# Kernel optimization log

Measured on AMD Instinct MI355X. Metric: run time of the kernel, lower is better.

The kernel has to match this reference:

```python
import jax, jax.numpy as jnp
import numpy as np

T, B, U, A, H, K, G = 800, 128, 64, 64, 256, 10, 20
IN1, IN2, IN3 = 3 + A, 3 + A + H, 3 + A + H


def _lstm_cell(x, h, c, W_ih, W_hh, b):
    # PyTorch LSTMCell: gates in order i, f, g, o
    z = x @ W_ih.T + h @ W_hh.T + b
    i, f, g, o = jnp.split(z, 4, axis=-1)
    c_new = jax.nn.sigmoid(f) * c + jax.nn.sigmoid(i) * jnp.tanh(g)
    h_new = jax.nn.sigmoid(o) * jnp.tanh(c_new)
    return h_new, c_new


def setup_inputs() -> dict:
    key = jax.random.key(0)
    ks = jax.random.split(key, 32)
    s = 0.08
    p = {}
    p['x'] = jax.random.normal(ks[0], (T, B, 3), jnp.float32)
    p['c'] = jax.random.uniform(ks[1], (B, U, A), jnp.float32)
    p['W1_ih'] = jax.random.normal(ks[2], (4 * H, IN1), jnp.float32) * s
    p['W1_hh'] = jax.random.normal(ks[3], (4 * H, H), jnp.float32) * s
    p['b1'] = jax.random.normal(ks[4], (4 * H,), jnp.float32) * s
    p['W2_ih'] = jax.random.normal(ks[5], (4 * H, IN2), jnp.float32) * s
    p['W2_hh'] = jax.random.normal(ks[6], (4 * H, H), jnp.float32) * s
    p['b2'] = jax.random.normal(ks[7], (4 * H,), jnp.float32) * s
    p['W3_ih'] = jax.random.normal(ks[8], (4 * H, IN3), jnp.float32) * s
    p['W3_hh'] = jax.random.normal(ks[9], (4 * H, H), jnp.float32) * s
    p['b3'] = jax.random.normal(ks[10], (4 * H,), jnp.float32) * s
    p['Ww'] = jax.random.normal(ks[11], (3 * K, H), jnp.float32) * s
    p['bw'] = jax.random.normal(ks[12], (3 * K,), jnp.float32) * s
    p['We'] = jax.random.normal(ks[13], (1, H), jnp.float32) * s
    p['be'] = jax.random.normal(ks[14], (1,), jnp.float32) * s
    p['Wpi'] = jax.random.normal(ks[15], (G, H), jnp.float32) * s
    p['bpi'] = jax.random.normal(ks[16], (G,), jnp.float32) * s
    p['Wm1'] = jax.random.normal(ks[17], (G, H), jnp.float32) * s
    p['bm1'] = jax.random.normal(ks[18], (G,), jnp.float32) * s
    p['Wm2'] = jax.random.normal(ks[19], (G, H), jnp.float32) * s
    p['bm2'] = jax.random.normal(ks[20], (G,), jnp.float32) * s
    p['Ws1'] = jax.random.normal(ks[21], (G, H), jnp.float32) * s
    p['bs1'] = jax.random.normal(ks[22], (G,), jnp.float32) * s
    p['Ws2'] = jax.random.normal(ks[23], (G, H), jnp.float32) * s
    p['bs2'] = jax.random.normal(ks[24], (G,), jnp.float32) * s
    p['Wr'] = jax.random.normal(ks[25], (G, H), jnp.float32) * s
    p['br'] = jax.random.normal(ks[26], (G,), jnp.float32) * s
    return p


def reference(x, c, W1_ih, W1_hh, b1, W2_ih, W2_hh, b2, W3_ih, W3_hh, b3,
              Ww, bw, We, be, Wpi, bpi, Wm1, bm1, Wm2, bm2,
              Ws1, bs1, Ws2, bs2, Wr, br):
    u = jnp.arange(U, dtype=x.dtype)  # character positions

    def step(carry, x_t):
        h1, c1, h2, c2, h3, c3, w, kappa = carry
        h1, c1 = _lstm_cell(jnp.concatenate([x_t, w], 1), h1, c1, W1_ih, W1_hh, b1)
        win = jnp.exp(h1 @ Ww.T + bw)                     # [B, 3K]
        alpha, beta, k = jnp.split(win, 3, axis=1)
        kappa = 0.1 * k + kappa                           # [B, K]
        # Phi[b,u] = sum_k alpha * exp(-beta * (kappa - u)^2)
        d = kappa[:, None, :] - u[None, :, None]          # [B, U, K]
        phi = jnp.sum(alpha[:, None, :] * jnp.exp(-beta[:, None, :] * d * d), -1)  # [B, U]
        w = jnp.einsum('bu,bua->ba', phi, c)              # [B, A]
        h2, c2 = _lstm_cell(jnp.concatenate([x_t, w, h1], 1), h2, c2, W2_ih, W2_hh, b2)
        h3, c3 = _lstm_cell(jnp.concatenate([x_t, w, h2], 1), h3, c3, W3_ih, W3_hh, b3)
        return (h1, c1, h2, c2, h3, c3, w, kappa), h3

    z = jnp.zeros((B, H), x.dtype)
    init = (z, z, z, z, z, z, jnp.ones((B, A), x.dtype), jnp.zeros((B, K), x.dtype))
    _, out = jax.lax.scan(step, init, x)                  # out: [T, B, H]

    es = jax.nn.sigmoid(-(out @ We.T + be)).squeeze(-1)   # 1/(1+exp(z)) == sigmoid(-z)
    pis = jax.nn.softmax(out @ Wpi.T + bpi, axis=2)
    mu1s = out @ Wm1.T + bm1
    mu2s = out @ Wm2.T + bm2
    sigma1s = jnp.exp(out @ Ws1.T + bs1)
    sigma2s = jnp.exp(out @ Ws2.T + bs2)
    rhos = jnp.tanh(out @ Wr.T + br)
    return es, pis, mu1s, mu2s, sigma1s, sigma2s, rhos
```

## Files before the change

### kernel.cpp

```cpp
#include <hip/hip_runtime.h>
#include <utility>

#define TT 800
#define BB 128
#define HH 256
#define UU 64
#define AA 64
#define KK 10
#define GG 20
#define NWG 256
#define GB 32
#define NGRP 4

typedef float f32x4 __attribute__((ext_vector_type(4)));
typedef __bf16 bf16y8 __attribute__((ext_vector_type(8)));
typedef short bf16s8 __attribute__((ext_vector_type(8)));
typedef unsigned long long u64x2 __attribute__((ext_vector_type(2)));

__device__ __forceinline__ float bf2f(unsigned short u) {
  return __uint_as_float(((unsigned int)u) << 16);
}
__device__ __forceinline__ unsigned short f2bf(float f) {
  unsigned int x = __float_as_uint(f);
  x += 0x7FFFu + ((x >> 16) & 1u);
  return (unsigned short)(x >> 16);
}
__device__ __forceinline__ unsigned packf(float v) {
  unsigned short hi = f2bf(v);
  unsigned short lo = f2bf(v - bf2f(hi));
  return (unsigned)hi | ((unsigned)lo << 16);
}
__device__ __forceinline__ float unpackf(unsigned u) {
  return bf2f((unsigned short)(u & 0xFFFF)) + bf2f((unsigned short)(u >> 16));
}
__device__ __forceinline__ float sigm(float x) { return 1.0f / (1.0f + __expf(-x)); }
__device__ __forceinline__ float rin(const void* p, size_t i, bool f32) {
  return f32 ? ((const float*)p)[i] : bf2f(((const unsigned short*)p)[i]);
}
__device__ __forceinline__ bf16y8 ld8(const unsigned short* p) {
  return __builtin_bit_cast(bf16y8, *(const bf16s8*)p);
}

__device__ __forceinline__ unsigned ald(const unsigned* p) {
  return __hip_atomic_load(p, __ATOMIC_RELAXED, __HIP_MEMORY_SCOPE_AGENT);
}
__device__ __forceinline__ void ast(unsigned* p, unsigned v) {
  __hip_atomic_store(p, v, __ATOMIC_RELAXED, __HIP_MEMORY_SCOPE_AGENT);
}

__device__ __forceinline__ void ld16(u64x2& d, const unsigned* p) {
  asm volatile("global_load_dwordx4 %0, %1, off sc0 sc1" : "=v"(d) : "v"(p));
}
template <int N>
__device__ __forceinline__ void waitvm() {
  asm volatile("s_waitcnt vmcnt(%0)" :: "i"(N) : "memory");
  __builtin_amdgcn_sched_barrier(0);
}

template <typename F, int... I>
__device__ __forceinline__ void unroll_seq(F&& f, std::integer_sequence<int, I...>) {
  (f(std::integral_constant<int, I>{}), ...);
}


struct KArgs {
  const void* in[27];
  float* out;
  float* kappa;
  unsigned *xu;
  unsigned *wu;
  unsigned *h1[2], *h2[2], *h3[2];
  unsigned* bar;
};

__device__ void fillB(unsigned short* Bhi, unsigned short* Blo, const void* Wih,
                      const void* Whh, int KP, int ihCols, int ihEnd, int hhStart,
                      int q, int tid, bool f32) {
  int total = KP * 16;
  for (int idx = tid; idx < total; idx += 256) {
    int k = idx >> 4, n = idx & 15;
    int row = (n >> 2) * HH + q * 4 + (n & 3);
    float v = 0.f;
    if (k < 3) v = rin(Wih, (size_t)row * ihCols + k, f32);
    else if (k >= 8 && k < ihEnd) v = rin(Wih, (size_t)row * ihCols + (k - 5), f32);
    else if (k >= hhStart && k < hhStart + 256) v = rin(Whh, (size_t)row * HH + (k - hhStart), f32);
    unsigned short hi = f2bf(v);
    int a = ((k >> 3) * 16 + n) * 8 + (k & 7);
    Bhi[a] = hi;
    Blo[a] = f2bf(v - bf2f(hi));
  }
}

template <int KC, bool R3, int WB>
__device__ __forceinline__ void gate_mfma(
    const unsigned* __restrict__ xt, const unsigned* __restrict__ wu,
    const unsigned* __restrict__ r2, const unsigned* __restrict__ r3,
    const unsigned* __restrict__ dz,
    const unsigned short* __restrict__ Bhi, const unsigned short* __restrict__ Blo,
    const float* __restrict__ bias4, float& creg, unsigned* __restrict__ hout,
    int grp, int q, float* zls, int tid) {
  const int wave = tid >> 6, lane = tid & 63;
  if ((wave >> 1) != (WB >> 1)) return;
  const int wv = wave & 1;
  const int n15 = lane & 15, quad = lane >> 4;
  const int b = grp * GB + wv * 16 + n15;

  unsigned xv0 = 0, xv1 = 0, xv2 = 0;
  if (quad == 0) {
    xv0 = xt[b * 3 + 0];
    xv1 = xt[b * 3 + 1];
    xv2 = xt[b * 3 + 2];
  }
  asm volatile("" :: "v"(xv0), "v"(xv1), "v"(xv2));

  constexpr int DEP = 12;
  u64x2 buf[DEP][2];

  auto addr = [&](int kc) -> const unsigned* {
    const int k0 = kc * 32 + quad * 8;
    if (kc == 0 && quad == 0) return dz;
    if (k0 < 72) return wu + ((k0 - 8) >> 3) * 1024 + b * 8;
    if (k0 < 328) return r2 + ((k0 - 72) >> 3) * 1024 + b * 8;
    if (R3 && k0 < 584) return r3 + ((k0 - 328) >> 3) * 1024 + b * 8;
    return dz;
  };
  auto issue = [&](int kc, int slot) {
    const unsigned* p = addr(kc);
    ld16(buf[slot][0], p);
    ld16(buf[slot][1], p + 4);
  };

#pragma unroll
  for (int kc = 0; kc < DEP && kc < KC; ++kc) issue(kc, kc);

  f32x4 acc = {0.f, 0.f, 0.f, 0.f};

  unroll_seq([&](auto kcc) {
    constexpr int kc = decltype(kcc)::value;
    constexpr int end = (kc + DEP < KC) ? (kc + DEP) : KC;
    waitvm<2 * (end - kc - 1)>();
    u64x2* sp = buf[kc % DEP];
    unsigned long long s[4] = { sp[0][0], sp[0][1], sp[1][0], sp[1][1] };
    bf16s8 th, tl;
#pragma unroll
    for (int j = 0; j < 4; ++j) {
      unsigned lo32 = (unsigned)s[j], hi32 = (unsigned)(s[j] >> 32);
      th[2 * j] = (short)(lo32 & 0xFFFFu);     tl[2 * j] = (short)(lo32 >> 16);
      th[2 * j + 1] = (short)(hi32 & 0xFFFFu); tl[2 * j + 1] = (short)(hi32 >> 16);
    }
    if constexpr (kc == 0) {
      if (quad == 0) {
        th[0] = (short)(xv0 & 0xFFFFu); tl[0] = (short)(xv0 >> 16);
        th[1] = (short)(xv1 & 0xFFFFu); tl[1] = (short)(xv1 >> 16);
        th[2] = (short)(xv2 & 0xFFFFu); tl[2] = (short)(xv2 >> 16);
      }
    }
    bf16y8 ah = __builtin_bit_cast(bf16y8, th);
    bf16y8 al = __builtin_bit_cast(bf16y8, tl);
    const int boff = ((kc * 4 + quad) * 16 + n15) * 8;
    bf16y8 bh = ld8(Bhi + boff), bl = ld8(Blo + boff);
    acc = __builtin_amdgcn_mfma_f32_16x16x32_bf16(ah, bh, acc, 0, 0, 0);
    acc = __builtin_amdgcn_mfma_f32_16x16x32_bf16(ah, bl, acc, 0, 0, 0);
    acc = __builtin_amdgcn_mfma_f32_16x16x32_bf16(al, bh, acc, 0, 0, 0);
    if constexpr (kc + DEP < KC) issue(kc + DEP, kc % DEP);
  }, std::make_integer_sequence<int, KC>{});

  float* zw = zls + wave * (16 * 17);
#pragma unroll
  for (int r = 0; r < 4; ++r) zw[(quad * 4 + r) * 17 + n15] = acc[r];
  const int m = lane >> 2, j = lane & 3;
  const int hu = q * 4 + j;
  const int bb = grp * GB + wv * 16 + m;
  float zi = zw[m * 17 + (0 + j)]  + bias4[0];
  float zf = zw[m * 17 + (4 + j)]  + bias4[1];
  float zg = zw[m * 17 + (8 + j)]  + bias4[2];
  float zo = zw[m * 17 + (12 + j)] + bias4[3];
  float cn = sigm(zf) * creg + sigm(zi) * tanhf(zg);
  creg = cn;
  float hn = sigm(zo) * tanhf(cn);
  ast(hout + (hu >> 3) * 1024 + bb * 8 + (hu & 7), packf(hn));
}

template <bool F32>
__device__ void window_stage(const KArgs& a, int b, const unsigned* __restrict__ h1c,
                             int tid, float* misc) {
  float* slab = misc;
  float* part = misc + 264;
  float* win  = misc + 508;
  float* kap  = misc + 538;
  float* phi  = misc + 552;
  const int wave = tid >> 6, lane = tid & 63;
  if (wave == 0) {
    const unsigned* p = h1c + (lane >> 1) * 1024 + b * 8 + (lane & 1) * 4;
    u64x2 d;
    ld16(d, p);
    waitvm<0>();
    const int hu0 = (lane >> 1) * 8 + (lane & 1) * 4;
    float* s4 = slab + (hu0 >> 5) * 33 + (hu0 & 31);
    s4[0] = unpackf((unsigned)d[0]);
    s4[1] = unpackf((unsigned)(d[0] >> 32));
    s4[2] = unpackf((unsigned)d[1]);
    s4[3] = unpackf((unsigned)(d[1] >> 32));
  }
  __syncthreads();
  if (tid < 240) {
    int r = tid >> 3, pp = tid & 7;
    const float* hh = slab + pp * 33;
    float s = 0.f;
    if (F32) {
      const f32x4* w4 = (const f32x4*)((const float*)a.in[11] + (size_t)r * HH + pp * 32);
#pragma unroll
      for (int j = 0; j < 8; ++j) {
        f32x4 v = w4[j];
        s += v[0] * hh[4 * j];     s += v[1] * hh[4 * j + 1];
        s += v[2] * hh[4 * j + 2]; s += v[3] * hh[4 * j + 3];
      }
    } else {
      const unsigned short* wr = (const unsigned short*)a.in[11] + (size_t)r * HH + pp * 32;
#pragma unroll
      for (int j = 0; j < 4; ++j) {
        bf16s8 v = *(const bf16s8*)(wr + 8 * j);
#pragma unroll
        for (int e = 0; e < 8; ++e) s += bf2f((unsigned short)v[e]) * hh[8 * j + e];
      }
    }
    part[tid] = s;
  }
  __syncthreads();
  if (tid < 30) {
    float s = rin(a.in[12], tid, F32);
#pragma unroll
    for (int i = 0; i < 8; ++i) s += part[tid * 8 + i];
    win[tid] = __expf(s);
  }
  __syncthreads();
  if (tid < 10) {
    float kp = a.kappa[b * KK + tid] + 0.1f * win[20 + tid];
    a.kappa[b * KK + tid] = kp;
    kap[tid] = kp;
  }
  __syncthreads();
  if (tid < 64) {
    float u = (float)tid, s = 0.f;
#pragma unroll
    for (int r = 0; r < 10; ++r) {
      float d = kap[r] - u;
      s += win[r] * __expf(-win[10 + r] * d * d);
    }
    phi[tid] = s;
  }
  __syncthreads();
  if (tid < 64) {
    float s = 0.f;
    for (int u = 0; u < 64; ++u) s += phi[u] * rin(a.in[1], ((size_t)b * UU + u) * AA + tid, F32);
    ast(a.wu + (tid >> 3) * 1024 + b * 8 + (tid & 7), packf(s));
  }
}

template <bool F32>
__device__ void proj_stage(const KArgs& a, int tt, const unsigned* __restrict__ h3b,
                           int b, int tid, float* misc) {
  float* shm  = misc;
  float* part = misc + 256;
  float* zp   = misc + 500;
  const int wave = tid >> 6, lane = tid & 63;
  if (wave == 0) {
    const unsigned* p = h3b + (lane >> 1) * 1024 + b * 8 + (lane & 1) * 4;
    u64x2 d;
    ld16(d, p);
    waitvm<0>();
    const int hu0 = (lane >> 1) * 8 + (lane & 1) * 4;
    shm[hu0 + 0] = unpackf((unsigned)d[0]);
    shm[hu0 + 1] = unpackf((unsigned)(d[0] >> 32));
    shm[hu0 + 2] = unpackf((unsigned)d[1]);
    shm[hu0 + 3] = unpackf((unsigned)(d[1] >> 32));
  }
  __syncthreads();
  if (tid < 242) {
    int o = tid >> 1, hf = tid & 1;
    const void* Wt;
    const void* bt;
    int rr;
    if (o == 0) {
      Wt = a.in[13]; bt = a.in[14]; rr = 0;
    } else {
      int fam = (o - 1) / 20;
      rr = (o - 1) % 20;
      Wt = a.in[15 + fam * 2];
      bt = a.in[16 + fam * 2];
    }
    float s0 = hf ? 0.f : rin(bt, rr, F32), s1 = 0.f;
    const float* hh = shm + hf * 128;
    if (F32) {
      const f32x4* w4 = (const f32x4*)((const float*)Wt + (size_t)rr * HH + hf * 128);
#pragma unroll 8
      for (int j = 0; j < 32; ++j) {
        f32x4 v = w4[j];
        s0 += v[0] * hh[4 * j];     s1 += v[1] * hh[4 * j + 1];
        s0 += v[2] * hh[4 * j + 2]; s1 += v[3] * hh[4 * j + 3];
      }
    } else {
      const unsigned short* wr = (const unsigned short*)Wt + (size_t)rr * HH + hf * 128;
#pragma unroll 4
      for (int j = 0; j < 16; ++j) {
        bf16s8 v = *(const bf16s8*)(wr + 8 * j);
#pragma unroll
        for (int e = 0; e < 8; e += 2) {
          s0 += bf2f((unsigned short)v[e]) * hh[8 * j + e];
          s1 += bf2f((unsigned short)v[e + 1]) * hh[8 * j + e + 1];
        }
      }
    }
    part[tid] = s0 + s1;
  }
  __syncthreads();
  if (tid < 121) zp[tid] = part[tid * 2] + part[tid * 2 + 1];
  __syncthreads();
  size_t tb = (size_t)tt * BB + b;
  if (tid == 0) {
    a.out[tb] = 1.f / (1.f + __expf(zp[0]));
  } else if (tid < 121) {
    int fam = (tid - 1) / 20, g = (tid - 1) % 20;
    float z = zp[tid];
    float val;
    if (fam == 0) {
      float mx = -1e30f;
      for (int jj = 0; jj < 20; ++jj) mx = fmaxf(mx, zp[1 + jj]);
      float den = 0.f;
      for (int jj = 0; jj < 20; ++jj) den += __expf(zp[1 + jj] - mx);
      val = __expf(z - mx) / den;
    } else if (fam <= 2) {
      val = z;
    } else if (fam <= 4) {
      val = __expf(z);
    } else {
      val = tanhf(z);
    }
    a.out[(size_t)102400 + (size_t)fam * 2048000 + tb * GG + g] = val;
  }
}

#define BAR_WORDS (256 + NWG * 32)

__global__ void __launch_bounds__(256) bar_init_kernel(unsigned* bar) {
  for (int i = threadIdx.x; i < BAR_WORDS; i += 256) bar[i] = 0u;
}

__global__ void __launch_bounds__(256, 1) hsm_kernel(KArgs a) {
  __shared__ unsigned short B1h[5632], B1l[5632];
  __shared__ unsigned short B2h[9728], B2l[9728];
  __shared__ unsigned short B3h[9728], B3l[9728];
  __shared__ float zls[4 * 16 * 17];
  __shared__ float misc[768];
  __shared__ unsigned islast;

  const int tid = threadIdx.x;
  const int wg = blockIdx.x;
  const int grp = wg >> 6;
  const int q = wg & 63;
  unsigned* cnt_full = a.bar;
  unsigned* cnt_grp  = a.bar + 32 * (1 + grp);
  unsigned* flags    = a.bar + 256;
  unsigned* myflag   = flags + wg * 32;
  const unsigned* dz = a.bar + 160;

  auto barrier = [&](unsigned* cnt, unsigned target, unsigned fv, int nfl, int flbase) {
    __syncthreads();
    if (tid == 0) {
      unsigned old = __hip_atomic_fetch_add(cnt, 1u, __ATOMIC_RELAXED,
                                            __HIP_MEMORY_SCOPE_AGENT);
      islast = (old == target - 1u) ? 1u : 0u;
    }
    __syncthreads();
    if (islast) {
      if (tid < nfl) ast(flags + (flbase + tid) * 32, fv);
    } else if (tid == 0) {
      while (ald(myflag) < fv) __builtin_amdgcn_s_sleep(2);
    }
    __syncthreads();
  };

  bool isf32;
  {
    const unsigned short* w = (const unsigned short*)a.in[3];
    int cnt = 0;
    for (int i = 0; i < 128; ++i) {
      float v = bf2f(w[i]);
      if (!(fabsf(v) <= 100.f)) cnt++;
    }
    isf32 = (cnt > 0);
  }

  const int g0 = wg * 256 + tid, gs = 65536;
  if (isf32) {
    const float* xp = (const float*)a.in[0];
    for (int i = g0; i < 307200; i += gs) ast(a.xu + i, packf(xp[i]));
  } else {
    const unsigned short* xp = (const unsigned short*)a.in[0];
    for (int i = g0; i < 307200; i += gs) ast(a.xu + i, (unsigned)xp[i]);
  }
  if (g0 < 32768) {
    ast(a.h1[0] + g0, 0u); ast(a.h1[1] + g0, 0u);
    ast(a.h2[0] + g0, 0u); ast(a.h2[1] + g0, 0u);
    ast(a.h3[0] + g0, 0u); ast(a.h3[1] + g0, 0u);
  }
  if (g0 < 8192) ast(a.wu + g0, 0x00003F80u);
  if (q < GB && tid < KK) a.kappa[(grp * GB + q) * KK + tid] = 0.f;

  float bs1[4], bs2[4], bs3[4];
  {
    const int hu = q * 4 + (tid & 3);
#pragma unroll
    for (int g = 0; g < 4; ++g) {
      bs1[g] = rin(a.in[4], g * HH + hu, isf32);
      bs2[g] = rin(a.in[7], g * HH + hu, isf32);
      bs3[g] = rin(a.in[10], g * HH + hu, isf32);
    }
  }
  float c1r = 0.f, c2r = 0.f, c3r = 0.f;

  fillB(B1h, B1l, a.in[2], a.in[3], 352, 67, 72, 72, q, tid, isf32);
  fillB(B2h, B2l, a.in[5], a.in[6], 608, 323, 328, 328, q, tid, isf32);
  fillB(B3h, B3l, a.in[8], a.in[9], 608, 323, 328, 328, q, tid, isf32);
  barrier(cnt_full, NWG, 1, NWG, 0);

  unsigned ph = 0;

  gate_mfma<11, false, 2>(a.xu, a.wu, a.h1[0], nullptr, dz, B1h, B1l, bs1, c1r,
                          a.h1[1], grp, q, zls, tid);
  ++ph; barrier(cnt_grp, ph * 64u, ph + 1u, 64, grp * 64);

  for (int t = 0; t < TT; ++t) {
    const int p = t & 1;
    const unsigned* xt = a.xu + (size_t)t * BB * 3;
    if (q < GB) {
      if (isf32) window_stage<true>(a, grp * GB + q, a.h1[1 - p], tid, misc);
      else       window_stage<false>(a, grp * GB + q, a.h1[1 - p], tid, misc);
    } else if (t > 0) {
      if (isf32) proj_stage<true>(a, t - 1, a.h3[p], grp * GB + q - GB, tid, misc);
      else       proj_stage<false>(a, t - 1, a.h3[p], grp * GB + q - GB, tid, misc);
    }
    ++ph; barrier(cnt_grp, ph * 64u, ph + 1u, 64, grp * 64);
    gate_mfma<19, true, 0>(xt, a.wu, a.h1[1 - p], a.h2[p], dz, B2h, B2l,
                           bs2, c2r, a.h2[1 - p], grp, q, zls, tid);
    ++ph; barrier(cnt_grp, ph * 64u, ph + 1u, 64, grp * 64);
    gate_mfma<19, true, 0>(xt, a.wu, a.h2[1 - p], a.h3[p], dz, B3h, B3l,
                           bs3, c3r, a.h3[1 - p], grp, q, zls, tid);
    if (t < TT - 1) {
      gate_mfma<11, false, 2>(xt + BB * 3, a.wu, a.h1[1 - p], nullptr, dz,
                              B1h, B1l, bs1, c1r, a.h1[p], grp, q, zls, tid);
    }
    ++ph; barrier(cnt_grp, ph * 64u, ph + 1u, 64, grp * 64);
  }
  if (q >= GB) {
    if (isf32) proj_stage<true>(a, TT - 1, a.h3[0], grp * GB + q - GB, tid, misc);
    else       proj_stage<false>(a, TT - 1, a.h3[0], grp * GB + q - GB, tid, misc);
  }
}

extern "C" void kernel_launch(void* const* d_in, const int* in_sizes, int n_in,
                              void* d_out, int out_size, void* d_ws, size_t ws_size,
                              hipStream_t stream) {
  KArgs a;
  for (int i = 0; i < 27; ++i) a.in[i] = d_in[i];
  a.out = (float*)d_out;

  char* ws = (char*)d_ws;
  size_t off = 0;
  auto take = [&](size_t bytes) {
    void* p = ws + off;
    off = (off + bytes + 127) & ~(size_t)127;
    return p;
  };
  a.kappa = (float*)take(1280 * 4);
  a.wu    = (unsigned*)take(8192 * 4);
  a.h1[0] = (unsigned*)take(32768 * 4);
  a.h1[1] = (unsigned*)take(32768 * 4);
  a.h2[0] = (unsigned*)take(32768 * 4);
  a.h2[1] = (unsigned*)take(32768 * 4);
  a.h3[0] = (unsigned*)take(32768 * 4);
  a.h3[1] = (unsigned*)take(32768 * 4);
  a.xu    = (unsigned*)take(307200 * 4);
  a.bar   = (unsigned*)take(BAR_WORDS * 4);

  bar_init_kernel<<<1, 256, 0, stream>>>(a.bar);
  hsm_kernel<<<NWG, 256, 0, stream>>>(a);
}
```

Baseline: 12.71 ms.

## Replace group barrier before layer-2 gates with per-window-block flag waits

Window blocks now publish a per-block step flag once they finish computing w. The layer-2 gate routine becomes a variant that first prefetches the h1 and h2 operand chunks, then spins only on the 32 window flags of its group before loading the w-dependent chunks. This removes one full group barrier per timestep and overlaps the h1/h2 loads with the wait. The cost is more polling traffic on the flags and a flag area added to the barrier buffer. Proj-stage blocks are no longer fenced at this point, so correctness depends on layer 2 not reading their outputs.

```diff
diff --git a/kernel.cpp b/kernel.cpp
--- a/kernel.cpp
+++ b/kernel.cpp
@@ -163,6 +163,114 @@
     acc = __builtin_amdgcn_mfma_f32_16x16x32_bf16(ah, bl, acc, 0, 0, 0);
     acc = __builtin_amdgcn_mfma_f32_16x16x32_bf16(al, bh, acc, 0, 0, 0);
     if constexpr (kc + DEP < KC) issue(kc + DEP, kc % DEP);
+  }, std::make_integer_sequence<int, KC>{});
+
+  float* zw = zls + wave * (16 * 17);
+#pragma unroll
+  for (int r = 0; r < 4; ++r) zw[(quad * 4 + r) * 17 + n15] = acc[r];
+  const int m = lane >> 2, j = lane & 3;
+  const int hu = q * 4 + j;
+  const int bb = grp * GB + wv * 16 + m;
+  float zi = zw[m * 17 + (0 + j)]  + bias4[0];
+  float zf = zw[m * 17 + (4 + j)]  + bias4[1];
+  float zg = zw[m * 17 + (8 + j)]  + bias4[2];
+  float zo = zw[m * 17 + (12 + j)] + bias4[3];
+  float cn = sigm(zf) * creg + sigm(zi) * tanhf(zg);
+  creg = cn;
+  float hn = sigm(zo) * tanhf(cn);
+  ast(hout + (hu >> 3) * 1024 + bb * 8 + (hu & 7), packf(hn));
+}
+
+template <int kc> constexpr int lw_wait() {
+  return kc == 0 ? 4 : kc == 1 ? 2 : kc == 2 ? 0 :
+         kc == 15 ? 6 : kc == 16 ? 4 : kc == 17 ? 2 : kc == 18 ? 0 : -1;
+}
+__device__ __forceinline__ void gate_mfma_lw(
+    const unsigned* __restrict__ xt, const unsigned* __restrict__ wu,
+    const unsigned* __restrict__ r2, const unsigned* __restrict__ r3,
+    const unsigned* __restrict__ dz,
+    const unsigned short* __restrict__ Bhi, const unsigned short* __restrict__ Blo,
+    const float* __restrict__ bias4, float& creg, unsigned* __restrict__ hout,
+    const unsigned* __restrict__ afl, unsigned tgt,
+    int grp, int q, float* zls, int tid) {
+  constexpr int KC = 19, DEP = 12;
+  const int wave = tid >> 6, lane = tid & 63;
+  if (wave >= 2) return;
+  const int wv = wave & 1;
+  const int n15 = lane & 15, quad = lane >> 4;
+  const int b = grp * GB + wv * 16 + n15;
+
+  unsigned xv0 = 0, xv1 = 0, xv2 = 0;
+  if (quad == 0) {
+    xv0 = xt[b * 3 + 0];
+    xv1 = xt[b * 3 + 1];
+    xv2 = xt[b * 3 + 2];
+  }
+  asm volatile("" :: "v"(xv0), "v"(xv1), "v"(xv2));
+
+  u64x2 buf[DEP][2];
+  u64x2 wbuf[3][2];
+
+  auto addr = [&](int kc) -> const unsigned* {
+    const int k0 = kc * 32 + quad * 8;
+    if (kc == 0 && quad == 0) return dz;
+    if (k0 < 72) return wu + ((k0 - 8) >> 3) * 1024 + b * 8;
+    if (k0 < 328) return r2 + ((k0 - 72) >> 3) * 1024 + b * 8;
+    if (k0 < 584) return r3 + ((k0 - 328) >> 3) * 1024 + b * 8;
+    return dz;
+  };
+  auto issue = [&](int kc, int slot) {
+    const unsigned* p = addr(kc);
+    ld16(buf[slot][0], p);
+    ld16(buf[slot][1], p + 4);
+  };
+
+#pragma unroll
+  for (int kc = 3; kc < 15; ++kc) issue(kc, kc % DEP);
+
+  {
+    const unsigned* fp = afl + (lane & 31) * 32;
+    unsigned v = ald(fp);
+    while (v < tgt) { __builtin_amdgcn_s_sleep(1); v = ald(fp); }
+  }
+
+#pragma unroll
+  for (int kc = 0; kc < 3; ++kc) {
+    const unsigned* p = addr(kc);
+    ld16(wbuf[kc][0], p);
+    ld16(wbuf[kc][1], p + 4);
+  }
+
+  f32x4 acc = {0.f, 0.f, 0.f, 0.f};
+
+  unroll_seq([&](auto kcc) {
+    constexpr int kc = decltype(kcc)::value;
+    constexpr int wn = lw_wait<kc>();
+    if constexpr (wn >= 0) waitvm<wn>();
+    u64x2* sp = (kc < 3) ? wbuf[kc] : buf[kc % DEP];
+    unsigned long long s[4] = { sp[0][0], sp[0][1], sp[1][0], sp[1][1] };
+    bf16s8 th, tl;
+#pragma unroll
+    for (int j = 0; j < 4; ++j) {
+      unsigned lo32 = (unsigned)s[j], hi32 = (unsigned)(s[j] >> 32);
+      th[2 * j] = (short)(lo32 & 0xFFFFu);     tl[2 * j] = (short)(lo32 >> 16);
+      th[2 * j + 1] = (short)(hi32 & 0xFFFFu); tl[2 * j + 1] = (short)(hi32 >> 16);
+    }
+    if constexpr (kc == 0) {
+      if (quad == 0) {
+        th[0] = (short)(xv0 & 0xFFFFu); tl[0] = (short)(xv0 >> 16);
+        th[1] = (short)(xv1 & 0xFFFFu); tl[1] = (short)(xv1 >> 16);
+        th[2] = (short)(xv2 & 0xFFFFu); tl[2] = (short)(xv2 >> 16);
+      }
+    }
+    bf16y8 ah = __builtin_bit_cast(bf16y8, th);
+    bf16y8 al = __builtin_bit_cast(bf16y8, tl);
+    const int boff = ((kc * 4 + quad) * 16 + n15) * 8;
+    bf16y8 bh = ld8(Bhi + boff), bl = ld8(Blo + boff);
+    acc = __builtin_amdgcn_mfma_f32_16x16x32_bf16(ah, bh, acc, 0, 0, 0);
+    acc = __builtin_amdgcn_mfma_f32_16x16x32_bf16(ah, bl, acc, 0, 0, 0);
+    acc = __builtin_amdgcn_mfma_f32_16x16x32_bf16(al, bh, acc, 0, 0, 0);
+    if constexpr (kc >= 3 && kc + DEP < KC) issue(kc + DEP, kc % DEP);
   }, std::make_integer_sequence<int, KC>{});
 
   float* zw = zls + wave * (16 * 17);
@@ -340,7 +448,7 @@
   }
 }
 
-#define BAR_WORDS (256 + NWG * 32)
+#define BAR_WORDS (256 + NWG * 32 + 4096)
 
 __global__ void __launch_bounds__(256) bar_init_kernel(unsigned* bar) {
   for (int i = threadIdx.x; i < BAR_WORDS; i += 256) bar[i] = 0u;
@@ -363,6 +471,8 @@
   unsigned* flags    = a.bar + 256;
   unsigned* myflag   = flags + wg * 32;
   const unsigned* dz = a.bar + 160;
+  unsigned* afl = a.bar + 256 + NWG * 32 + grp * 32 * 32;
+  unsigned* mya = afl + q * 32;
 
   auto barrier = [&](unsigned* cnt, unsigned target, unsigned fv, int nfl, int flbase) {
     __syncthreads();
@@ -436,13 +546,14 @@
     if (q < GB) {
       if (isf32) window_stage<true>(a, grp * GB + q, a.h1[1 - p], tid, misc);
       else       window_stage<false>(a, grp * GB + q, a.h1[1 - p], tid, misc);
+      __syncthreads();
+      if (tid == 0) ast(mya, (unsigned)(t + 1));
     } else if (t > 0) {
       if (isf32) proj_stage<true>(a, t - 1, a.h3[p], grp * GB + q - GB, tid, misc);
       else       proj_stage<false>(a, t - 1, a.h3[p], grp * GB + q - GB, tid, misc);
     }
-    ++ph; barrier(cnt_grp, ph * 64u, ph + 1u, 64, grp * 64);
-    gate_mfma<19, true, 0>(xt, a.wu, a.h1[1 - p], a.h2[p], dz, B2h, B2l,
-                           bs2, c2r, a.h2[1 - p], grp, q, zls, tid);
+    gate_mfma_lw(xt, a.wu, a.h1[1 - p], a.h2[p], dz, B2h, B2l,
+                 bs2, c2r, a.h2[1 - p], afl, (unsigned)(t + 1), grp, q, zls, tid);
     ++ph; barrier(cnt_grp, ph * 64u, ph + 1u, 64, grp * 64);
     gate_mfma<19, true, 0>(xt, a.wu, a.h2[1 - p], a.h3[p], dz, B3h, B3l,
                            bs3, c3r, a.h3[1 - p], grp, q, zls, tid);
```

New measurement: 12.50 ms. No clear change (-1.6%).
